# Kernel optimization log

Measured on AMD Instinct MI355X. Metric: run time of the kernel, lower is better.

The kernel has to match this reference:

```python
import jax, jax.numpy as jnp
import numpy as np

NUM_CLASSES = 6     # terrain classes 0..5
NUM_SUBJECTS = 16   # subject ids 0..15
MARGIN = 1.0
EPS = 1e-6          # torch pairwise_distance eps (added to the difference)


def setup_inputs() -> dict:
    key = jax.random.key(0)
    k1, k2, k3 = jax.random.split(key, 3)
    B, D = 131072, 256
    emb = jax.random.normal(k1, (B, D), dtype=jnp.float32)
    labels = jax.random.randint(k2, (B,), 0, NUM_CLASSES)
    sbj = jax.random.randint(k3, (B,), 0, NUM_SUBJECTS)
    return {"emb": emb, "labels": labels, "sbj": sbj}


def reference(emb, labels, sbj):
    """Within-subject hard-negative triplet loss.

    For every (subject s, class c) group with >=2 positives and >=1 negative
    (negatives = same subject, different class):
      anchor = first positive (in batch order), positive = second positive,
      negative = hardest (closest to anchor) same-subject other-class sample.
    Loss = mean over valid triplets of relu(d(a,p) - d(a,n) + margin), p=2.
    """
    B, D = emb.shape
    # flat grid of all (subject, class) pairs: P = NUM_SUBJECTS * NUM_CLASSES
    s_grid = jnp.repeat(jnp.arange(NUM_SUBJECTS), NUM_CLASSES)
    c_grid = jnp.tile(jnp.arange(NUM_CLASSES), NUM_SUBJECTS)

    def per_pair(s, c):
        m_pos = (sbj == s) & (labels == c)          # (B,)
        m_neg = (sbj == s) & (labels != c)          # (B,)
        cs = jnp.cumsum(m_pos)
        anchor_idx = jnp.argmax(m_pos & (cs == 1))  # first positive in batch order
        pos_idx = jnp.argmax(m_pos & (cs == 2))     # second positive
        valid = (jnp.sum(m_pos) >= 2) & (jnp.sum(m_neg) >= 1)
        return anchor_idx, pos_idx, m_neg, valid

    anchor_idx, pos_idx, m_neg, valid = jax.vmap(per_pair)(s_grid, c_grid)

    a = emb[anchor_idx]                              # (P, D)
    # squared L2 distance from each anchor to every sample (for mining only;
    # argmin of squared distance == argmin of distance, matching torch.cdist)
    d2 = (jnp.sum(a * a, axis=-1)[:, None]
          + jnp.sum(emb * emb, axis=-1)[None, :]
          - 2.0 * (a @ emb.T))                       # (P, B)
    d2 = jnp.where(m_neg, d2, jnp.inf)
    neg_idx = jnp.argmin(d2, axis=1)                 # (P,) hardest negative

    p = emb[pos_idx]                                 # (P, D)
    n = emb[neg_idx]                                 # (P, D)
    # torch TripletMarginLoss uses pairwise_distance: ||x1 - x2 + eps||_2
    d_ap = jnp.linalg.norm(a - p + EPS, axis=-1)
    d_an = jnp.linalg.norm(a - n + EPS, axis=-1)
    per_triplet = jnp.maximum(d_ap - d_an + MARGIN, 0.0)

    vf = valid.astype(emb.dtype)
    cnt = jnp.sum(vf)
    loss = jnp.sum(per_triplet * vf) / jnp.maximum(cnt, 1.0)
    return jnp.where(cnt > 0, loss, jnp.zeros((), emb.dtype))
```

## Files before the change

kernel.cpp:

```cpp
#include <hip/hip_runtime.h>

#define NUM_CLASSES 6
#define NUM_SUBJECTS 16
#define NUM_PAIRS (NUM_CLASSES * NUM_SUBJECTS)
#define MARGIN 1.0f
#define EPS 1e-6f
#define INF_I 0x7fffffff

typedef _Float16 h2_t __attribute__((ext_vector_type(2)));


__device__ __forceinline__ float wredsum(float v) {
#pragma unroll
    for (int m = 32; m >= 1; m >>= 1) v += __shfl_xor(v, m, 64);
    return v;
}

__device__ __forceinline__ unsigned int fkey(float f) {
    unsigned int b = __float_as_uint(f);
    return (b & 0x80000000u) ? ~b : (b | 0x80000000u);
}

__device__ __forceinline__ h2_t pk16(float x, float y) {
    return __builtin_bit_cast(h2_t, __builtin_amdgcn_cvt_pkrtz(x, y));
}

__global__ void k_init(int* min1, int* min2, int* cntPos, int* cntSbj,
                       unsigned long long* best, float* a2) {
    int t = threadIdx.x;
    if (t < NUM_PAIRS) {
        min1[t] = INF_I;
        min2[t] = INF_I;
        cntPos[t] = 0;
        best[t] = ~0ull;
        a2[t] = 0.f;
    }
    if (t < NUM_SUBJECTS) cntSbj[t] = 0;
}

__global__ __launch_bounds__(1024) void k_stats(const int* __restrict__ labels,
                                                const int* __restrict__ sbj,
                                                int* min1, int* min2, int* cntPos,
                                                int* cntSbj, int B) {
    __shared__ int l1[NUM_PAIRS], l2[NUM_PAIRS], lcp[NUM_PAIRS], lcs[NUM_SUBJECTS];
    for (int t = threadIdx.x; t < NUM_PAIRS; t += blockDim.x) { l1[t] = INF_I; l2[t] = INF_I; lcp[t] = 0; }
    if (threadIdx.x < NUM_SUBJECTS) lcs[threadIdx.x] = 0;
    __syncthreads();
    for (int i = blockIdx.x * blockDim.x + threadIdx.x; i < B; i += gridDim.x * blockDim.x) {
        int s = sbj[i], c = labels[i];
        int p = s * NUM_CLASSES + c;
        int o = atomicMin(&l1[p], i);
        atomicMin(&l2[p], max(o, i));
        atomicAdd(&lcp[p], 1);
        atomicAdd(&lcs[s], 1);
    }
    __syncthreads();
    for (int t = threadIdx.x; t < NUM_PAIRS; t += blockDim.x) {
        int m1 = l1[t];
        if (m1 != INF_I) {
            int o = atomicMin(&min1[t], m1);
            atomicMin(&min2[t], max(o, m1));
            if (l2[t] != INF_I) atomicMin(&min2[t], l2[t]);
            atomicAdd(&cntPos[t], lcp[t]);
        }
    }
    if (threadIdx.x < NUM_SUBJECTS && lcs[threadIdx.x]) atomicAdd(&cntSbj[threadIdx.x], lcs[threadIdx.x]);
}

__global__ void k_gather(const float4* __restrict__ emb4, const int* __restrict__ min1,
                         float4* anchors4, float* a2, int B) {
    int p = blockIdx.x;
    int lane = threadIdx.x;
    int idx = min1[p];
    if (idx < 0 || idx >= B) idx = 0;
    float4 v = emb4[(size_t)idx * 64 + lane];
    anchors4[(size_t)p * 64 + lane] = v;
    float t = v.x * v.x + v.y * v.y + v.z * v.z + v.w * v.w;
    t = wredsum(t);
    if (lane == 0) a2[p] = t;
}

__global__ __launch_bounds__(512, 6) void k_mine(const float4* __restrict__ emb4,
                                                 const int* __restrict__ labels,
                                                 const int* __restrict__ sbj,
                                                 const float4* __restrict__ anchors4,
                                                 const float* __restrict__ a2,
                                                 unsigned long long* gbest, int B) {
    __shared__ unsigned long long ancB[NUM_SUBJECTS * 385];
    __shared__ float a2l[NUM_PAIRS];
    __shared__ unsigned long long lbest[NUM_PAIRS];

    for (int u = threadIdx.x; u < NUM_PAIRS * 64; u += blockDim.x) {
        int row = u >> 6;
        int e = u & 63;
        float4 v = anchors4[u];
        unsigned int lou = __builtin_bit_cast(unsigned int, pk16(v.x, v.y));
        unsigned int hiu = __builtin_bit_cast(unsigned int, pk16(v.z, v.w));
        int s = row / NUM_CLASSES, c = row - s * NUM_CLASSES;
        ancB[s * 385 + c * 64 + e] = (unsigned long long)lou | ((unsigned long long)hiu << 32);
    }
    for (int t = threadIdx.x; t < NUM_PAIRS; t += blockDim.x) {
        a2l[t] = a2[t];
        lbest[t] = ~0ull;
    }
    __syncthreads();

    const int lane = threadIdx.x & 63;
    const int q = lane & 15;
    const int sloc = lane >> 4;
    const int wv = (int)(threadIdx.x >> 6);
    const int waveGlob = (int)blockIdx.x * 8 + wv;
    const int nwv = (int)gridDim.x * 8;

    for (int base = waveGlob * 4; base < B; base += nwv * 4) {
        int row = base + sloc;
        bool valid = row < B;
        int ic = valid ? row : (B - 1);
        int s = sbj[ic];
        int lbl = labels[ic];
        const float4* rp = emb4 + (size_t)ic * 64 + q;
        const unsigned long long* anc = ancB + s * 385 + q;

        float e2 = 0.f, d0 = 0.f, d1 = 0.f, d2v = 0.f, d3 = 0.f, d4 = 0.f, d5 = 0.f;
#pragma unroll
        for (int k = 0; k < 4; ++k) {
            float4 v = rp[k * 16];
            e2 = fmaf(v.x, v.x, fmaf(v.y, v.y, fmaf(v.z, v.z, fmaf(v.w, v.w, e2))));
            h2_t vlo = pk16(v.x, v.y);
            h2_t vhi = pk16(v.z, v.w);
            unsigned long long A;
            h2_t alo, ahi;
#if __has_builtin(__builtin_amdgcn_fdot2)
#define DOT(C, ACC)                                                              \
            A = anc[(C) * 64 + k * 16];                                          \
            alo = __builtin_bit_cast(h2_t, (unsigned int)A);                     \
            ahi = __builtin_bit_cast(h2_t, (unsigned int)(A >> 32));             \
            ACC = __builtin_amdgcn_fdot2(alo, vlo,                               \
                  __builtin_amdgcn_fdot2(ahi, vhi, ACC, false), false);
#else
#define DOT(C, ACC)                                                              \
            A = anc[(C) * 64 + k * 16];                                          \
            alo = __builtin_bit_cast(h2_t, (unsigned int)A);                     \
            ahi = __builtin_bit_cast(h2_t, (unsigned int)(A >> 32));             \
            ACC = fmaf((float)alo.x, v.x, fmaf((float)alo.y, v.y,                \
                  fmaf((float)ahi.x, v.z, fmaf((float)ahi.y, v.w, ACC))));
#endif
            DOT(0, d0) DOT(1, d1) DOT(2, d2v) DOT(3, d3) DOT(4, d4) DOT(5, d5)
#undef DOT
        }
#pragma unroll
        for (int m = 1; m <= 8; m <<= 1) {
            e2  += __shfl_xor(e2, m, 64);
            d0  += __shfl_xor(d0, m, 64);
            d1  += __shfl_xor(d1, m, 64);
            d2v += __shfl_xor(d2v, m, 64);
            d3  += __shfl_xor(d3, m, 64);
            d4  += __shfl_xor(d4, m, 64);
            d5  += __shfl_xor(d5, m, 64);
        }

        if (valid && q == 0) {
            int pb = s * NUM_CLASSES;
            float dc[NUM_CLASSES] = {d0, d1, d2v, d3, d4, d5};
#pragma unroll
            for (int c = 0; c < NUM_CLASSES; ++c) {
                if (c != lbl) {
                    float dd = a2l[pb + c] + e2 - 2.f * dc[c];
                    unsigned long long pk =
                        ((unsigned long long)fkey(dd) << 32) | (unsigned int)row;
                    atomicMin(&lbest[pb + c], pk);
                }
            }
        }
    }
    __syncthreads();
    for (int t = threadIdx.x; t < NUM_PAIRS; t += blockDim.x) {
        unsigned long long v = lbest[t];
        if (v != ~0ull) {
            unsigned long long cur = gbest[t];
            if (v < cur) atomicMin(&gbest[t], v);
        }
    }
}

__global__ __launch_bounds__(1024) void k_finalize(const float4* __restrict__ emb4,
                                                   const int* __restrict__ min1,
                                                   const int* __restrict__ min2,
                                                   const int* __restrict__ cntPos,
                                                   const int* __restrict__ cntSbj,
                                                   const unsigned long long* __restrict__ best,
                                                   float* out, int B) {
    __shared__ float vals[NUM_PAIRS];
    __shared__ int vld[NUM_PAIRS];
    int wave = threadIdx.x >> 6;
    int lane = threadIdx.x & 63;
    for (int p = wave; p < NUM_PAIRS; p += (blockDim.x >> 6)) {
        int s = p / NUM_CLASSES;
        int ai = min1[p], pi = min2[p];
        int npos = cntPos[p];
        int nneg = cntSbj[s] - npos;
        unsigned long long bb = best[p];
        int ni = (int)(bb & 0xffffffffu);
        bool ok = (npos >= 2) && (nneg >= 1) && (bb != ~0ull);
        if (ai < 0 || ai >= B) ai = 0;
        if (pi < 0 || pi >= B) pi = 0;
        if (ni < 0 || ni >= B) ni = 0;
        float4 a = emb4[(size_t)ai * 64 + lane];
        float4 pp = emb4[(size_t)pi * 64 + lane];
        float4 nn = emb4[(size_t)ni * 64 + lane];
        float dap = 0.f, dan = 0.f, t;
        t = a.x - pp.x + EPS; dap += t * t;
        t = a.y - pp.y + EPS; dap += t * t;
        t = a.z - pp.z + EPS; dap += t * t;
        t = a.w - pp.w + EPS; dap += t * t;
        t = a.x - nn.x + EPS; dan += t * t;
        t = a.y - nn.y + EPS; dan += t * t;
        t = a.z - nn.z + EPS; dan += t * t;
        t = a.w - nn.w + EPS; dan += t * t;
        dap = wredsum(dap);
        dan = wredsum(dan);
        if (lane == 0) {
            float lv = sqrtf(dap) - sqrtf(dan) + MARGIN;
            vals[p] = ok ? fmaxf(lv, 0.f) : 0.f;
            vld[p] = ok ? 1 : 0;
        }
    }
    __syncthreads();
    if (threadIdx.x == 0) {
        float sum = 0.f;
        int cnt = 0;
        for (int p = 0; p < NUM_PAIRS; ++p) { sum += vals[p]; cnt += vld[p]; }
        out[0] = (cnt > 0) ? (sum / (float)cnt) : 0.f;
    }
}

extern "C" void kernel_launch(void* const* d_in, const int* in_sizes, int n_in,
                              void* d_out, int out_size, void* d_ws, size_t ws_size,
                              hipStream_t stream) {
    const float* emb = (const float*)d_in[0];
    const int* labels = (const int*)d_in[1];
    const int* sbj = (const int*)d_in[2];
    float* out = (float*)d_out;
    const int B = in_sizes[1];
    const float4* emb4 = (const float4*)emb;

    char* ws = (char*)d_ws;
    int* min1 = (int*)(ws + 0);
    int* min2 = (int*)(ws + 384);
    int* cntPos = (int*)(ws + 768);
    int* cntSbj = (int*)(ws + 1152);
    unsigned long long* best = (unsigned long long*)(ws + 1216);
    float* a2 = (float*)(ws + 1984);
    float4* anchors4 = (float4*)(ws + 2432);

    k_init<<<1, 128, 0, stream>>>(min1, min2, cntPos, cntSbj, best, a2);

    k_stats<<<128, 1024, 0, stream>>>(labels, sbj, min1, min2, cntPos, cntSbj, B);

    k_gather<<<NUM_PAIRS, 64, 0, stream>>>(emb4, min1, anchors4, a2, B);

    k_mine<<<1024, 512, 0, stream>>>(emb4, labels, sbj, anchors4, a2, best, B);

    k_finalize<<<1, 1024, 0, stream>>>(emb4, min1, min2, cntPos, cntSbj, best, out, B);
}
```

Measured before the change: 71.66 us.

## Fuse finalize into mining kernel and pre-pack swizzled fp16 anchors in gather

The gather kernel now converts anchors to packed fp16 and writes them in a swizzled layout, so the mining kernel only copies a ready-made table into shared memory with 16-byte loads and reads two anchors per ulonglong2 LDS access. The anchor-norm term is dropped from the mining key because it is constant per pair and does not change the argmin. The finalize kernel is merged into the mining kernel's last block through a done-counter, which removes one launch. Launch bounds change from 6 to 4 waves per SIMD, which may reduce occupancy but allows more registers.

```diff
diff --git a/kernel.cpp b/kernel.cpp
--- a/kernel.cpp
+++ b/kernel.cpp
@@ -10,12 +10,6 @@
 typedef _Float16 h2_t __attribute__((ext_vector_type(2)));
 
 
-__device__ __forceinline__ float wredsum(float v) {
-#pragma unroll
-    for (int m = 32; m >= 1; m >>= 1) v += __shfl_xor(v, m, 64);
-    return v;
-}
-
 __device__ __forceinline__ unsigned int fkey(float f) {
     unsigned int b = __float_as_uint(f);
     return (b & 0x80000000u) ? ~b : (b | 0x80000000u);
@@ -25,17 +19,30 @@
     return __builtin_bit_cast(h2_t, __builtin_amdgcn_cvt_pkrtz(x, y));
 }
 
+__device__ __forceinline__ float dot4(unsigned long long A, h2_t vlo, h2_t vhi, float acc) {
+#if __has_builtin(__builtin_amdgcn_fdot2)
+    acc = __builtin_amdgcn_fdot2(__builtin_bit_cast(h2_t, (unsigned int)A), vlo, acc, false);
+    acc = __builtin_amdgcn_fdot2(__builtin_bit_cast(h2_t, (unsigned int)(A >> 32)), vhi, acc, false);
+#else
+    h2_t a = __builtin_bit_cast(h2_t, (unsigned int)A);
+    h2_t b = __builtin_bit_cast(h2_t, (unsigned int)(A >> 32));
+    acc = fmaf((float)a.x, (float)vlo.x, fmaf((float)a.y, (float)vlo.y,
+          fmaf((float)b.x, (float)vhi.x, fmaf((float)b.y, (float)vhi.y, acc))));
+#endif
+    return acc;
+}
+
 __global__ void k_init(int* min1, int* min2, int* cntPos, int* cntSbj,
-                       unsigned long long* best, float* a2) {
+                       unsigned long long* best, int* done) {
     int t = threadIdx.x;
     if (t < NUM_PAIRS) {
         min1[t] = INF_I;
         min2[t] = INF_I;
         cntPos[t] = 0;
         best[t] = ~0ull;
-        a2[t] = 0.f;
     }
     if (t < NUM_SUBJECTS) cntSbj[t] = 0;
+    if (t == 127) *done = 0;
 }
 
 __global__ __launch_bounds__(1024) void k_stats(const int* __restrict__ labels,
@@ -68,41 +75,43 @@
 }
 
 __global__ void k_gather(const float4* __restrict__ emb4, const int* __restrict__ min1,
-                         float4* anchors4, float* a2, int B) {
-    int p = blockIdx.x;
-    int lane = threadIdx.x;
-    int idx = min1[p];
+                         unsigned long long* ancT, int B) {
+    int pr = blockIdx.x;
+    int l = threadIdx.x;
+    int idx = min1[pr];
     if (idx < 0 || idx >= B) idx = 0;
-    float4 v = emb4[(size_t)idx * 64 + lane];
-    anchors4[(size_t)p * 64 + lane] = v;
-    float t = v.x * v.x + v.y * v.y + v.z * v.z + v.w * v.w;
-    t = wredsum(t);
-    if (lane == 0) a2[p] = t;
-}
-
-__global__ __launch_bounds__(512, 6) void k_mine(const float4* __restrict__ emb4,
+    float4 v = emb4[(size_t)idx * 64 + l];
+    unsigned int lou = __builtin_bit_cast(unsigned int, pk16(v.x, v.y));
+    unsigned int hiu = __builtin_bit_cast(unsigned int, pk16(v.z, v.w));
+    unsigned long long u = (unsigned long long)lou | ((unsigned long long)hiu << 32);
+    int s = pr / NUM_CLASSES, c = pr - s * NUM_CLASSES;
+    int q = l & 15, k = l >> 4;
+    int sw = ((2 * q + (k >> 1)) ^ (q >> 2)) * 2 + (k & 1);
+    ancT[s * 385 + c * 64 + sw] = u;
+}
+
+__global__ __launch_bounds__(512, 4) void k_mine(const float4* __restrict__ emb4,
                                                  const int* __restrict__ labels,
                                                  const int* __restrict__ sbj,
-                                                 const float4* __restrict__ anchors4,
-                                                 const float* __restrict__ a2,
-                                                 unsigned long long* gbest, int B) {
-    __shared__ unsigned long long ancB[NUM_SUBJECTS * 385];
-    __shared__ float a2l[NUM_PAIRS];
+                                                 const unsigned long long* __restrict__ ancT,
+                                                 unsigned long long* gbest,
+                                                 const int* __restrict__ min1,
+                                                 const int* __restrict__ min2,
+                                                 const int* __restrict__ cntPos,
+                                                 const int* __restrict__ cntSbj,
+                                                 int* done, float* out, int B) {
+    __shared__ __align__(16) unsigned long long ancB[NUM_SUBJECTS * 385];
     __shared__ unsigned long long lbest[NUM_PAIRS];
-
-    for (int u = threadIdx.x; u < NUM_PAIRS * 64; u += blockDim.x) {
-        int row = u >> 6;
-        int e = u & 63;
-        float4 v = anchors4[u];
-        unsigned int lou = __builtin_bit_cast(unsigned int, pk16(v.x, v.y));
-        unsigned int hiu = __builtin_bit_cast(unsigned int, pk16(v.z, v.w));
-        int s = row / NUM_CLASSES, c = row - s * NUM_CLASSES;
-        ancB[s * 385 + c * 64 + e] = (unsigned long long)lou | ((unsigned long long)hiu << 32);
-    }
-    for (int t = threadIdx.x; t < NUM_PAIRS; t += blockDim.x) {
-        a2l[t] = a2[t];
-        lbest[t] = ~0ull;
-    }
+    __shared__ float vals[NUM_PAIRS];
+    __shared__ int vld[NUM_PAIRS];
+    __shared__ int lastFlag;
+
+    {
+        const ulonglong2* src = (const ulonglong2*)ancT;
+        ulonglong2* dst = (ulonglong2*)ancB;
+        for (int u = threadIdx.x; u < NUM_SUBJECTS * 385 / 2; u += blockDim.x) dst[u] = src[u];
+    }
+    for (int t = threadIdx.x; t < NUM_PAIRS; t += blockDim.x) lbest[t] = ~0ull;
     __syncthreads();
 
     const int lane = threadIdx.x & 63;
@@ -111,6 +120,8 @@
     const int wv = (int)(threadIdx.x >> 6);
     const int waveGlob = (int)blockIdx.x * 8 + wv;
     const int nwv = (int)gridDim.x * 8;
+    const int p0 = ((2 * q) ^ (q >> 2)) * 2;
+    const int p1 = ((2 * q + 1) ^ (q >> 2)) * 2;
 
     for (int base = waveGlob * 4; base < B; base += nwv * 4) {
         int row = base + sloc;
@@ -119,55 +130,48 @@
         int s = sbj[ic];
         int lbl = labels[ic];
         const float4* rp = emb4 + (size_t)ic * 64 + q;
-        const unsigned long long* anc = ancB + s * 385 + q;
-
-        float e2 = 0.f, d0 = 0.f, d1 = 0.f, d2v = 0.f, d3 = 0.f, d4 = 0.f, d5 = 0.f;
-#pragma unroll
-        for (int k = 0; k < 4; ++k) {
-            float4 v = rp[k * 16];
-            e2 = fmaf(v.x, v.x, fmaf(v.y, v.y, fmaf(v.z, v.z, fmaf(v.w, v.w, e2))));
-            h2_t vlo = pk16(v.x, v.y);
-            h2_t vhi = pk16(v.z, v.w);
-            unsigned long long A;
-            h2_t alo, ahi;
-#if __has_builtin(__builtin_amdgcn_fdot2)
-#define DOT(C, ACC)                                                              \
-            A = anc[(C) * 64 + k * 16];                                          \
-            alo = __builtin_bit_cast(h2_t, (unsigned int)A);                     \
-            ahi = __builtin_bit_cast(h2_t, (unsigned int)(A >> 32));             \
-            ACC = __builtin_amdgcn_fdot2(alo, vlo,                               \
-                  __builtin_amdgcn_fdot2(ahi, vhi, ACC, false), false);
-#else
-#define DOT(C, ACC)                                                              \
-            A = anc[(C) * 64 + k * 16];                                          \
-            alo = __builtin_bit_cast(h2_t, (unsigned int)A);                     \
-            ahi = __builtin_bit_cast(h2_t, (unsigned int)(A >> 32));             \
-            ACC = fmaf((float)alo.x, v.x, fmaf((float)alo.y, v.y,                \
-                  fmaf((float)ahi.x, v.z, fmaf((float)ahi.y, v.w, ACC))));
-#endif
-            DOT(0, d0) DOT(1, d1) DOT(2, d2v) DOT(3, d3) DOT(4, d4) DOT(5, d5)
-#undef DOT
+        float4 v0 = rp[0], v1 = rp[16], v2 = rp[32], v3 = rp[48];
+
+        float e2 = 0.f;
+        e2 = fmaf(v0.x, v0.x, fmaf(v0.y, v0.y, fmaf(v0.z, v0.z, fmaf(v0.w, v0.w, e2))));
+        e2 = fmaf(v1.x, v1.x, fmaf(v1.y, v1.y, fmaf(v1.z, v1.z, fmaf(v1.w, v1.w, e2))));
+        e2 = fmaf(v2.x, v2.x, fmaf(v2.y, v2.y, fmaf(v2.z, v2.z, fmaf(v2.w, v2.w, e2))));
+        e2 = fmaf(v3.x, v3.x, fmaf(v3.y, v3.y, fmaf(v3.z, v3.z, fmaf(v3.w, v3.w, e2))));
+
+        h2_t vl0 = pk16(v0.x, v0.y), vh0 = pk16(v0.z, v0.w);
+        h2_t vl1 = pk16(v1.x, v1.y), vh1 = pk16(v1.z, v1.w);
+        h2_t vl2 = pk16(v2.x, v2.y), vh2 = pk16(v2.z, v2.w);
+        h2_t vl3 = pk16(v3.x, v3.y), vh3 = pk16(v3.z, v3.w);
+
+        const unsigned long long* anc = ancB + s * 385;
+        float d[NUM_CLASSES];
+#pragma unroll
+        for (int c = 0; c < NUM_CLASSES; ++c) {
+            const unsigned long long* ab = anc + c * 64;
+            ulonglong2 A01 = *(const ulonglong2*)(ab + p0);
+            ulonglong2 A23 = *(const ulonglong2*)(ab + p1);
+            float acc = 0.f;
+            acc = dot4(A01.x, vl0, vh0, acc);
+            acc = dot4(A01.y, vl1, vh1, acc);
+            acc = dot4(A23.x, vl2, vh2, acc);
+            acc = dot4(A23.y, vl3, vh3, acc);
+            d[c] = acc;
         }
 #pragma unroll
         for (int m = 1; m <= 8; m <<= 1) {
-            e2  += __shfl_xor(e2, m, 64);
-            d0  += __shfl_xor(d0, m, 64);
-            d1  += __shfl_xor(d1, m, 64);
-            d2v += __shfl_xor(d2v, m, 64);
-            d3  += __shfl_xor(d3, m, 64);
-            d4  += __shfl_xor(d4, m, 64);
-            d5  += __shfl_xor(d5, m, 64);
+            e2 += __shfl_xor(e2, m, 64);
+#pragma unroll
+            for (int c = 0; c < NUM_CLASSES; ++c) d[c] += __shfl_xor(d[c], m, 64);
         }
 
         if (valid && q == 0) {
             int pb = s * NUM_CLASSES;
-            float dc[NUM_CLASSES] = {d0, d1, d2v, d3, d4, d5};
 #pragma unroll
             for (int c = 0; c < NUM_CLASSES; ++c) {
                 if (c != lbl) {
-                    float dd = a2l[pb + c] + e2 - 2.f * dc[c];
+                    float kd = e2 - 2.f * d[c];
                     unsigned long long pk =
-                        ((unsigned long long)fkey(dd) << 32) | (unsigned int)row;
+                        ((unsigned long long)fkey(kd) << 32) | (unsigned int)row;
                     atomicMin(&lbest[pb + c], pk);
                 }
             }
@@ -181,33 +185,31 @@
             if (v < cur) atomicMin(&gbest[t], v);
         }
     }
-}
-
-__global__ __launch_bounds__(1024) void k_finalize(const float4* __restrict__ emb4,
-                                                   const int* __restrict__ min1,
-                                                   const int* __restrict__ min2,
-                                                   const int* __restrict__ cntPos,
-                                                   const int* __restrict__ cntSbj,
-                                                   const unsigned long long* __restrict__ best,
-                                                   float* out, int B) {
-    __shared__ float vals[NUM_PAIRS];
-    __shared__ int vld[NUM_PAIRS];
+    __threadfence();
+    if (threadIdx.x == 0) {
+        int old = atomicAdd(done, 1);
+        lastFlag = (old == (int)gridDim.x - 1);
+    }
+    __syncthreads();
+    if (!lastFlag) return;
+    __threadfence();
+
     int wave = threadIdx.x >> 6;
-    int lane = threadIdx.x & 63;
-    for (int p = wave; p < NUM_PAIRS; p += (blockDim.x >> 6)) {
+    int flane = threadIdx.x & 63;
+    for (int p = wave; p < NUM_PAIRS; p += 8) {
         int s = p / NUM_CLASSES;
         int ai = min1[p], pi = min2[p];
         int npos = cntPos[p];
         int nneg = cntSbj[s] - npos;
-        unsigned long long bb = best[p];
+        unsigned long long bb = atomicMin(&gbest[p], ~0ull);
         int ni = (int)(bb & 0xffffffffu);
         bool ok = (npos >= 2) && (nneg >= 1) && (bb != ~0ull);
         if (ai < 0 || ai >= B) ai = 0;
         if (pi < 0 || pi >= B) pi = 0;
         if (ni < 0 || ni >= B) ni = 0;
-        float4 a = emb4[(size_t)ai * 64 + lane];
-        float4 pp = emb4[(size_t)pi * 64 + lane];
-        float4 nn = emb4[(size_t)ni * 64 + lane];
+        float4 a = emb4[(size_t)ai * 64 + flane];
+        float4 pp = emb4[(size_t)pi * 64 + flane];
+        float4 nn = emb4[(size_t)ni * 64 + flane];
         float dap = 0.f, dan = 0.f, t;
         t = a.x - pp.x + EPS; dap += t * t;
         t = a.y - pp.y + EPS; dap += t * t;
@@ -217,9 +219,12 @@
         t = a.y - nn.y + EPS; dan += t * t;
         t = a.z - nn.z + EPS; dan += t * t;
         t = a.w - nn.w + EPS; dan += t * t;
-        dap = wredsum(dap);
-        dan = wredsum(dan);
-        if (lane == 0) {
+#pragma unroll
+        for (int m = 32; m >= 1; m >>= 1) {
+            dap += __shfl_xor(dap, m, 64);
+            dan += __shfl_xor(dan, m, 64);
+        }
+        if (flane == 0) {
             float lv = sqrtf(dap) - sqrtf(dan) + MARGIN;
             vals[p] = ok ? fmaxf(lv, 0.f) : 0.f;
             vld[p] = ok ? 1 : 0;
@@ -250,16 +255,15 @@
     int* cntPos = (int*)(ws + 768);
     int* cntSbj = (int*)(ws + 1152);
     unsigned long long* best = (unsigned long long*)(ws + 1216);
-    float* a2 = (float*)(ws + 1984);
-    float4* anchors4 = (float4*)(ws + 2432);
-
-    k_init<<<1, 128, 0, stream>>>(min1, min2, cntPos, cntSbj, best, a2);
+    int* done = (int*)(ws + 1984);
+    unsigned long long* ancT = (unsigned long long*)(ws + 2048);
+
+    k_init<<<1, 128, 0, stream>>>(min1, min2, cntPos, cntSbj, best, done);
 
     k_stats<<<128, 1024, 0, stream>>>(labels, sbj, min1, min2, cntPos, cntSbj, B);
 
-    k_gather<<<NUM_PAIRS, 64, 0, stream>>>(emb4, min1, anchors4, a2, B);
-
-    k_mine<<<1024, 512, 0, stream>>>(emb4, labels, sbj, anchors4, a2, best, B);
-
-    k_finalize<<<1, 1024, 0, stream>>>(emb4, min1, min2, cntPos, cntSbj, best, out, B);
-}
+    k_gather<<<NUM_PAIRS, 64, 0, stream>>>(emb4, min1, ancT, B);
+
+    k_mine<<<1024, 512, 0, stream>>>(emb4, labels, sbj, ancT, best,
+                                     min1, min2, cntPos, cntSbj, done, out, B);
+}
```

Measured after the change: 258.1 us. 260% more time.
